# Kernel optimization log

Measured on AMD Instinct MI355X. Metric: run time of the kernel, lower is better.

Reference implementation:

```python
import jax, jax.numpy as jnp
import numpy as np

CAT = 19          # category_num + 1 (last slot is the catch-all cluster)
ATT_SCALE = float(np.sqrt(200.0))


def _layernorm(x, scale, bias, eps=1e-5):
    mu = jnp.mean(x, axis=-1, keepdims=True)
    var = jnp.mean((x - mu) ** 2, axis=-1, keepdims=True)
    return (x - mu) * jax.lax.rsqrt(var + eps) * scale + bias


def setup_inputs() -> dict:
    key = jax.random.key(0)
    ks = jax.random.split(key, 16)
    B, N, H, D, A, L = 64, 16, 100, 400, 200, 2
    nodes = H + (CAT - 1)  # 118
    s = 1.0 / np.sqrt(D)
    return {
        "history_embedding": jax.random.normal(ks[0], (B, H, D), jnp.float32),
        "candidate_news_representation": jax.random.normal(ks[1], (B, N, D), jnp.float32),
        "user_history_graph": jax.random.uniform(ks[2], (B, nodes, nodes), jnp.float32) / nodes,
        "user_history_category_mask": jax.random.randint(ks[3], (B, CAT), 0, 2, jnp.int32),
        "user_history_category_indices": jax.random.randint(ks[4], (B, H), 0, CAT, jnp.int32),
        "proxy_node_embedding": jax.random.normal(ks[5], (CAT - 1, D), jnp.float32) * 0.02,
        "gcn_W": jax.random.normal(ks[6], (L, D, D), jnp.float32) * s,
        "gcn_b": jnp.zeros((L, D), jnp.float32),
        "ln_scale": jnp.ones((L, D), jnp.float32),
        "ln_bias": jnp.zeros((L, D), jnp.float32),
        "Kw": jax.random.normal(ks[7], (D, A), jnp.float32) * s,
        "Qw": jax.random.normal(ks[8], (D, A), jnp.float32) * s,
        "Qb": jnp.zeros((A,), jnp.float32),
        "affine_W": jax.random.normal(ks[9], (D, D), jnp.float32) * s,
        "affine_b": jnp.zeros((D,), jnp.float32),
        "icKw": jax.random.normal(ks[10], (D, A), jnp.float32) * s,
        "icQw": jax.random.normal(ks[11], (D, A), jnp.float32) * s,
        "icQb": jnp.zeros((A,), jnp.float32),
    }


def _forward(history_embedding, candidate_news_representation, user_history_graph,
             proxy_node_embedding, gcn_W, gcn_b, ln_scale, ln_bias,
             Kw, Qw, Qb, affine_W, affine_b, icKw, icQw, icQb,
             user_history_category_mask, user_history_category_indices):
    B, H, D = history_embedding.shape
    N = candidate_news_representation.shape[1]
    L = gcn_W.shape[0]

    # append proxy cluster nodes to the history graph nodes (dropout = identity at eval)
    he = jnp.concatenate(
        [history_embedding, jnp.broadcast_to(proxy_node_embedding[None], (B, CAT - 1, D))],
        axis=1)  # [B, 118, D]

    # GCN with residual + layernorm per layer, then global residual
    h = he
    for l in range(L):
        z = jnp.einsum('bij,bjd->bid', user_history_graph, h) @ gcn_W[l] + gcn_b[l]
        z = jax.nn.relu(z) + h
        h = _layernorm(z, ln_scale[l], ln_bias[l])
    gcn_feat = (h + he)[:, :H]  # [B, H, D]

    # intra-cluster scatter softmax over history items grouped by category
    K = gcn_feat @ Kw                                     # [B, H, A]
    Q = candidate_news_representation @ Qw + Qb           # [B, N, A]
    a = jnp.einsum('bha,bna->bnh', K, Q) / ATT_SCALE      # [B, N, H]

    onehot = jax.nn.one_hot(user_history_category_indices, CAT, dtype=a.dtype)  # [B, H, C]
    seg = onehot.astype(bool)
    neg = jnp.finfo(a.dtype).min
    # segment-max for stable softmax: [B, N, H, C] -> max over H
    seg_max = jnp.where(seg[:, None], a[..., None], neg).max(axis=2)            # [B, N, C]
    a_shift = a - jnp.einsum('bhc,bnc->bnh', onehot, seg_max)
    e = jnp.exp(a_shift)
    denom = jnp.einsum('bhc,bnc->bnh', onehot, jnp.einsum('bnh,bhc->bnc', e, onehot))
    alpha = e / denom                                                           # [B, N, H]

    # scatter-sum of attention-weighted gcn features into category clusters
    weighted = alpha[..., None] * gcn_feat[:, None]                             # [B, N, H, D]
    intra = jnp.einsum('bnhd,bhc->bncd', weighted, onehot)                      # [B, N, C, D]
    intra = jax.nn.relu(intra @ affine_W + affine_b) + intra

    # inter-cluster scaled-dot-product candidate attention (last cluster always valid)
    mask = user_history_category_mask.at[:, -1].set(1).astype(bool)[:, None, :]  # [B, 1, C]
    Kf = intra @ icKw                                                           # [B, N, C, A]
    q = candidate_news_representation @ icQw + icQb                             # [B, N, A]
    s = jnp.einsum('bnca,bna->bnc', Kf, q) / ATT_SCALE
    w = jax.nn.softmax(jnp.where(mask, s, neg), axis=-1)
    return jnp.einsum('bnc,bncd->bnd', w, intra)                                # [B, N, D]


def reference(history_embedding, candidate_news_representation, user_history_graph,
              user_history_category_mask, user_history_category_indices,
              proxy_node_embedding, gcn_W, gcn_b, ln_scale, ln_bias,
              Kw, Qw, Qb, affine_W, affine_b, icKw, icQw, icQb):
    return _forward(history_embedding, candidate_news_representation, user_history_graph,
                    proxy_node_embedding, gcn_W, gcn_b, ln_scale, ln_bias,
                    Kw, Qw, Qb, affine_W, affine_b, icKw, icQw, icQb,
                    user_history_category_mask, user_history_category_indices)
```

## Files before the change

### kernel.cpp

```cpp
#include <hip/hip_runtime.h>
#include <hip/hip_bf16.h>
#include <math.h>

#define BB 64
#define NN 16
#define HH 100
#define DD 400
#define AA 200
#define CATN 19
#define NODES 118
#define BN (BB*NODES)
#define BH (BB*HH)
#define ATT_INV 0.07071067811865475f

typedef __attribute__((ext_vector_type(4))) float f32x4;
typedef __attribute__((ext_vector_type(8))) short s16x8;

__device__ __forceinline__ unsigned short f2bf(float f) {
  union { float f; unsigned int u; } v; v.f = f;
  unsigned int r = v.u + 0x7FFFu + ((v.u >> 16) & 1u);
  return (unsigned short)(r >> 16);
}
__device__ __forceinline__ float bf2f(unsigned short u) {
  union { unsigned int i; float f; } v; v.i = ((unsigned int)u) << 16; return v.f;
}

__global__ __launch_bounds__(256) void k_toT_he(const float* __restrict__ hist,
    const float* __restrict__ proxy, float* __restrict__ he,
    unsigned short* __restrict__ T) {
  __shared__ float t_sh[64][129];
  const int b = blockIdx.x / 7, dt = blockIdx.x % 7;
  const int d0 = dt * 64;
  const int tid = threadIdx.x;
  const int dc = tid & 63, jr = tid >> 6;
  for (int j0 = 0; j0 < 128; j0 += 4) {
    int j = j0 + jr, d = d0 + dc;
    float v = 0.f;
    if (j < NODES && d < DD) {
      v = (j < HH) ? hist[((size_t)b * HH + j) * DD + d]
                   : proxy[(size_t)(j - HH) * DD + d];
      he[((size_t)b * NODES + j) * DD + d] = v;
    }
    t_sh[dc][j] = v;
  }
  __syncthreads();
  const int jc = tid & 127, dr2 = tid >> 7;
  for (int di = 0; di < 64; di += 2) {
    int dr = di + dr2;
    int d = d0 + dr;
    if (d < 416) T[((size_t)b * 416 + d) * 128 + jc] = f2bf(t_sh[dr][jc]);
  }
}

template<int RPB>
__global__ __launch_bounds__(256) void k_toT(const float* __restrict__ h,
    unsigned short* __restrict__ T) {
  __shared__ float t_sh[64][129];
  const int b = blockIdx.x / 7, dt = blockIdx.x % 7;
  const int d0 = dt * 64;
  const int tid = threadIdx.x;
  const int dc = tid & 63, jr = tid >> 6;
  for (int j0 = 0; j0 < 128; j0 += 4) {
    int j = j0 + jr, d = d0 + dc;
    float v = (j < RPB && d < DD) ? h[((size_t)b * RPB + j) * DD + d] : 0.f;
    t_sh[dc][j] = v;
  }
  __syncthreads();
  const int jc = tid & 127, dr2 = tid >> 7;
  for (int di = 0; di < 64; di += 2) {
    int dr = di + dr2;
    int d = d0 + dr;
    if (d < 416) T[((size_t)b * 416 + d) * 128 + jc] = f2bf(t_sh[dr][jc]);
  }
}

__global__ __launch_bounds__(256) void k_toT_gf(const float* __restrict__ h2,
    const float* __restrict__ he, float* __restrict__ gf,
    unsigned short* __restrict__ T) {
  __shared__ float t_sh[64][129];
  const int b = blockIdx.x / 7, dt = blockIdx.x % 7;
  const int d0 = dt * 64;
  const int tid = threadIdx.x;
  const int dc = tid & 63, jr = tid >> 6;
  for (int j0 = 0; j0 < 128; j0 += 4) {
    int j = j0 + jr, d = d0 + dc;
    float v = 0.f;
    if (j < HH && d < DD) {
      size_t src = ((size_t)b * NODES + j) * DD + d;
      v = h2[src] + he[src];
      gf[((size_t)b * HH + j) * DD + d] = v;
    }
    t_sh[dc][j] = v;
  }
  __syncthreads();
  const int jc = tid & 127, dr2 = tid >> 7;
  for (int di = 0; di < 64; di += 2) {
    int dr = di + dr2;
    int d = d0 + dr;
    if (d < 416) T[((size_t)b * 416 + d) * 128 + jc] = f2bf(t_sh[dr][jc]);
  }
}

__global__ __launch_bounds__(256) void k_gmm(const float* __restrict__ G,
    const unsigned short* __restrict__ hT, unsigned short* __restrict__ tmpb) {
  __shared__ unsigned short a_sh[16 * 136];
  const int tid = threadIdx.x;
  const int g = (blockIdx.x & 7) * (gridDim.x >> 3) + (blockIdx.x >> 3);
  const int b = g >> 3;
  const int i0 = (g & 7) * 16;
  for (int idx = tid; idx < 16 * 128; idx += 256) {
    int r = idx >> 7, j = idx & 127;
    int i = i0 + r;
    float v = (i < NODES && j < NODES) ? G[((size_t)b * NODES + i) * NODES + j] : 0.f;
    a_sh[r * 136 + j] = f2bf(v);
  }
  __syncthreads();
  const int lane = tid & 63, w = tid >> 6;
  const int lrow = lane & 15, lk = lane >> 4;
  const int cbeg = w * 7;
  f32x4 acc[7];
#pragma unroll
  for (int c = 0; c < 7; ++c) acc[c] = f32x4{0.f, 0.f, 0.f, 0.f};
  const unsigned short* ap = &a_sh[lrow * 136 + lk * 8];
  const unsigned short* wp = &hT[((size_t)b * 416 + cbeg * 16 + lrow) * 128 + lk * 8];
  for (int ks = 0; ks < 4; ++ks) {
    s16x8 af = *reinterpret_cast<const s16x8*>(ap + ks * 32);
#pragma unroll
    for (int c = 0; c < 7; ++c) {
      s16x8 bf = *reinterpret_cast<const s16x8*>(wp + (size_t)c * 16 * 128 + ks * 32);
      acc[c] = __builtin_amdgcn_mfma_f32_16x16x32_bf16(af, bf, acc[c], 0, 0, 0);
    }
  }
#pragma unroll
  for (int c = 0; c < 7; ++c) {
    int col = (cbeg + c) * 16 + lrow;
    if (col < 416) {
#pragma unroll
      for (int j = 0; j < 4; ++j) {
        int i = i0 + lk * 4 + j;
        if (i < NODES)
          tmpb[((size_t)b * NODES + i) * 416 + col] = f2bf(acc[c][j]);
      }
    }
  }
}

__global__ __launch_bounds__(256) void k_mgb_ln(
    const unsigned short* __restrict__ A, const unsigned short* __restrict__ Wt,
    const float* __restrict__ bias, const float* __restrict__ resid,
    const float* __restrict__ lns, const float* __restrict__ lnb,
    float* __restrict__ out) {
  __shared__ float ps_sh[16][4][2];
  const int tid = threadIdx.x;
  const int g = (blockIdx.x % 8) * (gridDim.x / 8) + blockIdx.x / 8;
  const size_t row0 = (size_t)g * 16;
  const int lane = tid & 63, w = tid >> 6;
  const int lrow = lane & 15, lk = lane >> 4;
  const int cbeg = w * 7;
  f32x4 acc[7];
#pragma unroll
  for (int c = 0; c < 7; ++c) acc[c] = f32x4{0.f, 0.f, 0.f, 0.f};
  const unsigned short* ap = &A[(row0 + lrow) * 416 + lk * 8];
  const unsigned short* wp = &Wt[((size_t)(cbeg * 16) + lrow) * 416 + lk * 8];
  for (int ks = 0; ks < 13; ++ks) {
    s16x8 af = *reinterpret_cast<const s16x8*>(ap + ks * 32);
#pragma unroll
    for (int c = 0; c < 7; ++c) {
      s16x8 bf = *reinterpret_cast<const s16x8*>(wp + (size_t)c * 16 * 416 + ks * 32);
      acc[c] = __builtin_amdgcn_mfma_f32_16x16x32_bf16(af, bf, acc[c], 0, 0, 0);
    }
  }
  float zs[4], zq[4];
#pragma unroll
  for (int j = 0; j < 4; ++j) { zs[j] = 0.f; zq[j] = 0.f; }
#pragma unroll
  for (int c = 0; c < 7; ++c) {
    int col = (cbeg + c) * 16 + lrow;
    bool cv = col < DD;
    float bv = cv ? bias[col] : 0.f;
#pragma unroll
    for (int j = 0; j < 4; ++j) {
      float z = 0.f;
      if (cv)
        z = fmaxf(acc[c][j] + bv, 0.f) + resid[(row0 + lk * 4 + j) * (size_t)DD + col];
      acc[c][j] = z;
      zs[j] += z;
      zq[j] += z * z;
    }
  }
#pragma unroll
  for (int j = 0; j < 4; ++j) {
    zs[j] += __shfl_xor(zs[j], 1, 64); zq[j] += __shfl_xor(zq[j], 1, 64);
    zs[j] += __shfl_xor(zs[j], 2, 64); zq[j] += __shfl_xor(zq[j], 2, 64);
    zs[j] += __shfl_xor(zs[j], 4, 64); zq[j] += __shfl_xor(zq[j], 4, 64);
    zs[j] += __shfl_xor(zs[j], 8, 64); zq[j] += __shfl_xor(zq[j], 8, 64);
  }
  if (lrow == 0) {
#pragma unroll
    for (int j = 0; j < 4; ++j) {
      ps_sh[lk * 4 + j][w][0] = zs[j];
      ps_sh[lk * 4 + j][w][1] = zq[j];
    }
  }
  __syncthreads();
  float mu[4], rs[4];
#pragma unroll
  for (int j = 0; j < 4; ++j) {
    int la = lk * 4 + j;
    float s = ps_sh[la][0][0] + ps_sh[la][1][0] + ps_sh[la][2][0] + ps_sh[la][3][0];
    float q = ps_sh[la][0][1] + ps_sh[la][1][1] + ps_sh[la][2][1] + ps_sh[la][3][1];
    mu[j] = s * (1.0f / DD);
    rs[j] = 1.0f / sqrtf(q * (1.0f / DD) - mu[j] * mu[j] + 1e-5f);
  }
#pragma unroll
  for (int c = 0; c < 7; ++c) {
    int col = (cbeg + c) * 16 + lrow;
    if (col < DD) {
      float sc = lns[col], bo = lnb[col];
#pragma unroll
      for (int j = 0; j < 4; ++j)
        out[(row0 + lk * 4 + j) * (size_t)DD + col] = (acc[c][j] - mu[j]) * rs[j] * sc + bo;
    }
  }
}

__global__ __launch_bounds__(256) void k_prep_all(const float* __restrict__ gW,
    const float* __restrict__ afW, const float* __restrict__ Kw,
    const float* __restrict__ Qw, const float* __restrict__ icQw,
    const float* __restrict__ icKw, const float* __restrict__ Qb,
    const float* __restrict__ icQb, unsigned short* __restrict__ wbase,
    float* __restrict__ bias3) {
  int idx = blockIdx.x * 256 + threadIdx.x;
  const int SG = 416 * 416;
  const int SK = 224 * 416;
  if (idx < SG) {
    int n = idx / 416, k = idx - n * 416;
    wbase[idx] = (n < 400 && k < 400) ? f2bf(gW[(size_t)k * 400 + n]) : (unsigned short)0;
    return;
  }
  idx -= SG;
  if (idx < SG) {
    int n = idx / 416, k = idx - n * 416;
    wbase[173056 + idx] = (n < 400 && k < 400) ? f2bf(gW[160000 + (size_t)k * 400 + n]) : (unsigned short)0;
    return;
  }
  idx -= SG;
  if (idx < SG) {
    int n = idx / 416, k = idx - n * 416;
    wbase[346112 + idx] = (n < 400 && k < 400) ? f2bf(afW[(size_t)k * 400 + n]) : (unsigned short)0;
    return;
  }
  idx -= SG;
  if (idx < SK) {
    int n = idx / 416, k = idx - n * 416;
    wbase[519168 + idx] = (n < 200 && k < 400) ? f2bf(Kw[(size_t)k * 200 + n]) : (unsigned short)0;
    return;
  }
  idx -= SK;
  if (idx < SK) {
    int d = idx / 224, a = idx - d * 224;
    wbase[612352 + idx] = (d < 400 && a < 200) ? f2bf(icKw[(size_t)d * 200 + a]) : (unsigned short)0;
    return;
  }
  idx -= SK;
  if (idx < SK) {
    int k = idx / 224, a = idx - k * 224;
    wbase[705536 + idx] = (k < 400 && a < 200) ? f2bf(icQw[(size_t)k * 200 + a]) : (unsigned short)0;
    return;
  }
  idx -= SK;
  if (idx < 208 * 416) {
    int n = idx / 416, k = idx - n * 416;
    wbase[798720 + idx] = (n < 200 && k < 400) ? f2bf(Qw[(size_t)k * 200 + n]) : (unsigned short)0;
    return;
  }
  idx -= 208 * 416;
  if (idx < 608) {
    float v = 0.f;
    if (idx < 200) v = Qb[idx];
    else if (idx >= 208) {
      const float* kr = icKw + (size_t)(idx - 208) * 200;
      float s = 0.f;
      for (int a = 0; a < 200; ++a) s += icQb[a] * kr[a];
      v = s;
    }
    bias3[idx] = v;
  }
}

__global__ __launch_bounds__(256) void k_prep_M(const unsigned short* __restrict__ icKwB,
    const unsigned short* __restrict__ icQwB, unsigned short* __restrict__ wqp) {
  const int tid = threadIdx.x;
  const size_t row0 = (size_t)blockIdx.x * 32;
  const int lane = tid & 63, w = tid >> 6;
  const int lrow = lane & 15, lk = lane >> 4;
  const int rg = w & 1, nh = w >> 1;
  const int cbeg = nh * 13;
  f32x4 acc[13];
#pragma unroll
  for (int c = 0; c < 13; ++c) acc[c] = f32x4{0.f, 0.f, 0.f, 0.f};
  const unsigned short* ap = &icKwB[(row0 + rg * 16 + lrow) * 224 + lk * 8];
  const unsigned short* bp = &icQwB[((size_t)(cbeg * 16) + lrow) * 224 + lk * 8];
  for (int ks = 0; ks < 7; ++ks) {
    s16x8 af = *reinterpret_cast<const s16x8*>(ap + ks * 32);
#pragma unroll
    for (int c = 0; c < 13; ++c) {
      s16x8 bf = *reinterpret_cast<const s16x8*>(bp + (size_t)c * 16 * 224 + ks * 32);
      acc[c] = __builtin_amdgcn_mfma_f32_16x16x32_bf16(af, bf, acc[c], 0, 0, 0);
    }
  }
  const int r0 = rg * 16 + lk * 4;
#pragma unroll
  for (int c = 0; c < 13; ++c) {
    int k = (cbeg + c) * 16 + lrow;
#pragma unroll
    for (int j = 0; j < 4; ++j) {
      size_t d = row0 + r0 + j;
      if (d < 400) wqp[(208 + d) * 416 + k] = f2bf(acc[c][j]);
    }
  }
}

template<int KDIM, int KPAD, int NOUT, int EPI>
__global__ __launch_bounds__(256) void k_mg(
    const float* __restrict__ A, const unsigned short* __restrict__ Wt,
    const float* __restrict__ bias, float* __restrict__ out, float* __restrict__ out2) {
  constexpr int APITCH = KPAD + 8;
  constexpr int NF = (NOUT + 15) / 16;
  constexpr int NF0 = (NF + 1) / 2;
  constexpr int KS = KPAD / 32;
  constexpr int E4 = KDIM / 4;
  constexpr int PADN = KPAD - KDIM;
  __shared__ unsigned short a_sh[32 * APITCH];
  const int tid = threadIdx.x;
  const int g = (blockIdx.x % 8) * (gridDim.x / 8) + blockIdx.x / 8;
  const size_t row0 = (size_t)g * 32;
  for (int i = tid; i < 32 * E4; i += 256) {
    int r = i / E4, c4 = i - r * E4;
    const float4 v = *reinterpret_cast<const float4*>(&A[(row0 + r) * (size_t)KDIM + c4 * 4]);
    unsigned int lo = (unsigned int)f2bf(v.x) | ((unsigned int)f2bf(v.y) << 16);
    unsigned int hi = (unsigned int)f2bf(v.z) | ((unsigned int)f2bf(v.w) << 16);
    *reinterpret_cast<uint2*>(&a_sh[r * APITCH + c4 * 4]) = make_uint2(lo, hi);
  }
  for (int i = tid; i < 32 * PADN; i += 256) {
    int r = i / PADN, c = i - r * PADN;
    a_sh[r * APITCH + KDIM + c] = 0;
  }
  __syncthreads();
  const int lane = tid & 63, w = tid >> 6;
  const int lrow = lane & 15, lk = lane >> 4;
  const int rg = w & 1, nh = w >> 1;
  const int cbeg = nh * NF0;
  f32x4 acc[NF0];
#pragma unroll
  for (int c = 0; c < NF0; ++c) acc[c] = f32x4{0.f, 0.f, 0.f, 0.f};
  const unsigned short* ap = &a_sh[(rg * 16 + lrow) * APITCH + lk * 8];
  const unsigned short* wp = &Wt[((size_t)(cbeg * 16) + lrow) * KPAD + lk * 8];
  for (int ks = 0; ks < KS; ++ks) {
    s16x8 af = *reinterpret_cast<const s16x8*>(ap + ks * 32);
#pragma unroll
    for (int c = 0; c < NF0; ++c) {
      s16x8 bf = *reinterpret_cast<const s16x8*>(wp + (size_t)c * 16 * KPAD + ks * 32);
      acc[c] = __builtin_amdgcn_mfma_f32_16x16x32_bf16(af, bf, acc[c], 0, 0, 0);
    }
  }
  const int r0 = rg * 16 + lk * 4;
  if (EPI == 0) {
#pragma unroll
    for (int c = 0; c < NF0; ++c) {
      int col = (cbeg + c) * 16 + lrow;
      if (col < NOUT) {
#pragma unroll
        for (int j = 0; j < 4; ++j)
          out[(row0 + r0 + j) * (size_t)NOUT + col] = acc[c][j];
      }
    }
  } else {
#pragma unroll
    for (int c = 0; c < NF0; ++c) {
      int col = (cbeg + c) * 16 + lrow;
      if (col < 200) {
        float bv = bias[col];
#pragma unroll
        for (int j = 0; j < 4; ++j)
          out[(row0 + r0 + j) * (size_t)AA + col] = acc[c][j] + bv;
      } else if (col >= 208 && col < 608) {
        float bv = bias[col];
#pragma unroll
        for (int j = 0; j < 4; ++j)
          out2[(row0 + r0 + j) * (size_t)DD + (col - 208)] = acc[c][j] + bv;
      }
    }
  }
}

__global__ __launch_bounds__(256) void k_palpha(const float* __restrict__ K,
    const float* __restrict__ Q, const int* __restrict__ cat,
    unsigned short* __restrict__ P) {
  __shared__ float q_sh[AA];
  __shared__ float a_sh[HH];
  __shared__ int c_sh[HH];
  __shared__ float smax[CATN], sden[CATN];
  const int i = blockIdx.x;
  const int xcd = i & 7, s = i >> 3;
  const int b = 8 * xcd + (s >> 4);
  const int n = s & 15;
  const int bn = b * 16 + n;
  const int tid = threadIdx.x;
  if (tid < AA) q_sh[tid] = Q[(size_t)bn * AA + tid];
  if (tid < HH) c_sh[tid] = cat[b * HH + tid];
  __syncthreads();
  if (tid < 2 * HH) {
    int h = tid >> 1, half = tid & 1;
    const float* kp = K + ((size_t)b * HH + h) * AA + half * 100;
    const float* qp = q_sh + half * 100;
    float sv = 0.f;
#pragma unroll 4
    for (int a = 0; a < 100; ++a) sv += kp[a] * qp[a];
    sv += __shfl_xor(sv, 1, 64);
    if (half == 0) a_sh[h] = sv * ATT_INV;
  }
  __syncthreads();
  if (tid < CATN) {
    float m = -3.4e38f;
    for (int h = 0; h < HH; ++h)
      if (c_sh[h] == tid) m = fmaxf(m, a_sh[h]);
    smax[tid] = m;
  }
  __syncthreads();
  if (tid < HH) a_sh[tid] = expf(a_sh[tid] - smax[c_sh[tid]]);
  __syncthreads();
  if (tid < CATN) {
    float dsum = 0.f;
    for (int h = 0; h < HH; ++h)
      if (c_sh[h] == tid) dsum += a_sh[h];
    sden[tid] = dsum;
  }
  __syncthreads();
  if (tid < HH) a_sh[tid] = a_sh[tid] / sden[c_sh[tid]];
  __syncthreads();
  for (int idx = tid; idx < CATN * 128; idx += 256) {
    int c = idx >> 7, h = idx & 127;
    float v = (h < HH && c_sh[h] == c) ? a_sh[h] : 0.f;
    P[((size_t)b * 320 + n * CATN + c) * 128 + h] = f2bf(v);
  }
}

__global__ __launch_bounds__(256) void k_sc(const unsigned short* __restrict__ P,
    const unsigned short* __restrict__ gfT, unsigned short* __restrict__ intraB) {
  const int i = blockIdx.x;
  const int xcd = i & 7, s = i >> 3;
  const int b = 8 * xcd + s / CATN;
  const int t = s % CATN;
  const int tid = threadIdx.x;
  const int lane = tid & 63, w = tid >> 6;
  const int lrow = lane & 15, lk = lane >> 4;
  const int cbeg = w * 7;
  f32x4 acc[7];
#pragma unroll
  for (int c = 0; c < 7; ++c) acc[c] = f32x4{0.f, 0.f, 0.f, 0.f};
  const unsigned short* ap = &P[((size_t)b * 320 + t * 16 + lrow) * 128 + lk * 8];
  const unsigned short* wp = &gfT[((size_t)b * 416 + cbeg * 16 + lrow) * 128 + lk * 8];
  for (int ks = 0; ks < 4; ++ks) {
    s16x8 af = *reinterpret_cast<const s16x8*>(ap + ks * 32);
#pragma unroll
    for (int c = 0; c < 7; ++c) {
      s16x8 bf = *reinterpret_cast<const s16x8*>(wp + (size_t)c * 16 * 128 + ks * 32);
      acc[c] = __builtin_amdgcn_mfma_f32_16x16x32_bf16(af, bf, acc[c], 0, 0, 0);
    }
  }
#pragma unroll
  for (int c = 0; c < 7; ++c) {
    int col = (cbeg + c) * 16 + lrow;
    if (col < 416) {
#pragma unroll
      for (int j = 0; j < 4; ++j)
        intraB[((size_t)b * 304 + t * 16 + lk * 4 + j) * 416 + col] =
            f2bf(col < DD ? acc[c][j] : 0.f);
    }
  }
}

__global__ __launch_bounds__(256) void k_afq(
    const unsigned short* __restrict__ A, const unsigned short* __restrict__ Wt,
    const float* __restrict__ bias, const float* __restrict__ p,
    float* __restrict__ s_pre, unsigned short* __restrict__ out2) {
  __shared__ float ps_sh[16][4];
  const int tid = threadIdx.x;
  const int g = (blockIdx.x % 8) * (gridDim.x / 8) + blockIdx.x / 8;
  const size_t row0 = (size_t)g * 16;
  const int lane = tid & 63, w = tid >> 6;
  const int lrow = lane & 15, lk = lane >> 4;
  const int cbeg = w * 7;
  f32x4 acc[7];
#pragma unroll
  for (int c = 0; c < 7; ++c) acc[c] = f32x4{0.f, 0.f, 0.f, 0.f};
  const unsigned short* ap = &A[(row0 + lrow) * 416 + lk * 8];
  const unsigned short* wp = &Wt[((size_t)(cbeg * 16) + lrow) * 416 + lk * 8];
  for (int ks = 0; ks < 13; ++ks) {
    s16x8 af = *reinterpret_cast<const s16x8*>(ap + ks * 32);
#pragma unroll
    for (int c = 0; c < 7; ++c) {
      s16x8 bf = *reinterpret_cast<const s16x8*>(wp + (size_t)c * 16 * 416 + ks * 32);
      acc[c] = __builtin_amdgcn_mfma_f32_16x16x32_bf16(af, bf, acc[c], 0, 0, 0);
    }
  }
  const float* prow[4];
#pragma unroll
  for (int j = 0; j < 4; ++j)
    prow[j] = p + (size_t)((row0 + lk * 4 + j) / CATN) * DD;
  float sp[4] = {0.f, 0.f, 0.f, 0.f};
#pragma unroll
  for (int c = 0; c < 7; ++c) {
    int col = (cbeg + c) * 16 + lrow;
    if (col < DD) {
      float bv = bias[col];
#pragma unroll
      for (int j = 0; j < 4; ++j) {
        size_t ra = row0 + lk * 4 + j;
        float v = fmaxf(acc[c][j] + bv, 0.f) + bf2f(A[ra * 416 + col]);
        out2[ra * 416 + col] = f2bf(v);
        sp[j] += v * prow[j][col];
      }
    }
  }
#pragma unroll
  for (int j = 0; j < 4; ++j) {
    sp[j] += __shfl_xor(sp[j], 1, 64);
    sp[j] += __shfl_xor(sp[j], 2, 64);
    sp[j] += __shfl_xor(sp[j], 4, 64);
    sp[j] += __shfl_xor(sp[j], 8, 64);
  }
  if (lrow == 0) {
#pragma unroll
    for (int j = 0; j < 4; ++j) ps_sh[lk * 4 + j][w] = sp[j];
  }
  __syncthreads();
  if (tid < 16)
    s_pre[row0 + tid] =
        (ps_sh[tid][0] + ps_sh[tid][1] + ps_sh[tid][2] + ps_sh[tid][3]) * ATT_INV;
}

__global__ __launch_bounds__(256) void k_final(const unsigned short* __restrict__ intra2B,
    const float* __restrict__ s_pre, const int* __restrict__ mask,
    float* __restrict__ out) {
  __shared__ float w_sh[CATN];
  const int i = blockIdx.x;
  const int xcd = i & 7, s = i >> 3;
  const int b = 8 * xcd + (s >> 4);
  const int n = s & 15;
  const int bn = b * 16 + n;
  const int tid = threadIdx.x;
  if (tid == 0) {
    float sv[CATN];
    float mx = -3.4e38f;
#pragma unroll
    for (int c = 0; c < CATN; ++c) {
      bool mk = (c == CATN - 1) || (mask[b * CATN + c] != 0);
      float sc = mk ? s_pre[bn * CATN + c] : -3.4e38f;
      sv[c] = sc;
      mx = fmaxf(mx, sc);
    }
    float den = 0.f;
#pragma unroll
    for (int c = 0; c < CATN; ++c) {
      float e = (sv[c] <= -3.3e38f) ? 0.f : expf(sv[c] - mx);
      w_sh[c] = e;
      den += e;
    }
    float inv = 1.0f / den;
#pragma unroll
    for (int c = 0; c < CATN; ++c) w_sh[c] *= inv;
  }
  __syncthreads();
  const unsigned short* ib = intra2B + (size_t)bn * CATN * 416;
  for (int d = tid; d < DD; d += 256) {
    float o = 0.f;
#pragma unroll
    for (int c = 0; c < CATN; ++c) o += w_sh[c] * bf2f(ib[c * 416 + d]);
    out[(size_t)bn * DD + d] = o;
  }
}

extern "C" void kernel_launch(void* const* d_in, const int* in_sizes, int n_in,
                              void* d_out, int out_size, void* d_ws, size_t ws_size,
                              hipStream_t stream) {
  const float* hist  = (const float*)d_in[0];
  const float* cand  = (const float*)d_in[1];
  const float* G     = (const float*)d_in[2];
  const int*   cmask = (const int*)d_in[3];
  const int*   cidx  = (const int*)d_in[4];
  const float* proxy = (const float*)d_in[5];
  const float* gW    = (const float*)d_in[6];
  const float* gb    = (const float*)d_in[7];
  const float* lns   = (const float*)d_in[8];
  const float* lnb   = (const float*)d_in[9];
  const float* Kw    = (const float*)d_in[10];
  const float* Qw    = (const float*)d_in[11];
  const float* Qbb   = (const float*)d_in[12];
  const float* afW   = (const float*)d_in[13];
  const float* afb   = (const float*)d_in[14];
  const float* icKw  = (const float*)d_in[15];
  const float* icQw  = (const float*)d_in[16];
  const float* icQb  = (const float*)d_in[17];
  float* out = (float*)d_out;
  float* ws  = (float*)d_ws;

  float* he    = ws;
  float* s1    = ws + 3020800;
  float* s2f   = ws + 6041600;
  unsigned short* tmpb   = (unsigned short*)(ws + 6041600);
  unsigned short* TB     = (unsigned short*)(ws + 9062400);
  unsigned short* intraB = (unsigned short*)(ws + 10766336);
  unsigned short* intra2B= (unsigned short*)(ws + 14813184);
  unsigned short* wbase  = (unsigned short*)(ws + 18860032);
  float* bias3 = ws + 19385856;
  unsigned short* Pbuf = (unsigned short*)ws;
  float* qbuf  = ws + 1310720;
  float* pbuf  = ws + 1515520;
  float* s_pre = ws + 1925120;
  float* Kbuf  = s1;
  unsigned short* gW0t  = wbase;
  unsigned short* gW1t  = wbase + 173056;
  unsigned short* afWt  = wbase + 346112;
  unsigned short* Kwt   = wbase + 519168;
  unsigned short* icKwB = wbase + 612352;
  unsigned short* icQwB = wbase + 705536;
  unsigned short* Wqp   = wbase + 798720;

  k_prep_all<<<3461, 256, 0, stream>>>(gW, afW, Kw, Qw, icQw, icKw, Qbb, icQb, wbase, bias3);
  k_prep_M<<<13, 256, 0, stream>>>(icKwB, icQwB, Wqp);
  k_toT_he<<<448, 256, 0, stream>>>(hist, proxy, he, TB);
  k_gmm<<<512, 256, 0, stream>>>(G, TB, tmpb);
  k_mgb_ln<<<BN / 16, 256, 0, stream>>>(tmpb, gW0t, gb, he, lns, lnb, s1);
  k_toT<NODES><<<448, 256, 0, stream>>>(s1, TB);
  k_gmm<<<512, 256, 0, stream>>>(G, TB, tmpb);
  k_mgb_ln<<<BN / 16, 256, 0, stream>>>(tmpb, gW1t, gb + DD, s1, lns + DD, lnb + DD, s1);
  k_toT_gf<<<448, 256, 0, stream>>>(s1, he, s2f, TB);
  k_mg<400, 416, 200, 0><<<BH / 32, 256, 0, stream>>>(s2f, Kwt, nullptr, Kbuf, nullptr);
  k_mg<400, 416, 608, 6><<<BB * NN / 32, 256, 0, stream>>>(cand, Wqp, bias3, qbuf, pbuf);
  k_palpha<<<BB * NN, 256, 0, stream>>>(Kbuf, qbuf, cidx, Pbuf);
  k_sc<<<BB * CATN, 256, 0, stream>>>(Pbuf, TB, intraB);
  k_afq<<<BB * NN * CATN / 16, 256, 0, stream>>>(intraB, afWt, afb, pbuf, s_pre, intra2B);
  k_final<<<BB * NN, 256, 0, stream>>>(intra2B, s_pre, cmask, out);
}
```

Measured before the change: 311.5 us.

## Fuse transposed bf16 writes into GCN LayerNorm epilogue; retile small GEMMs to 16 rows

Removes the standalone transpose kernels (k_toT, k_toT_gf). The LayerNorm GEMM epilogue now writes the transposed bf16 copy directly, and in the second layer also adds the residual to produce the graph features. The K/Q projection GEMMs switch to 16-row tiles with each wave owning a column slice, which doubles block count for better occupancy, and the padded weight tail is zero-filled. The fused transposed stores are scattered 2-byte writes with a stride of 128 elements, so they are poorly coalesced compared with the shared-memory transpose they replace.

```diff
diff --git a/kernel.cpp b/kernel.cpp
--- a/kernel.cpp
+++ b/kernel.cpp
@@ -52,55 +52,6 @@
   }
 }
 
-template<int RPB>
-__global__ __launch_bounds__(256) void k_toT(const float* __restrict__ h,
-    unsigned short* __restrict__ T) {
-  __shared__ float t_sh[64][129];
-  const int b = blockIdx.x / 7, dt = blockIdx.x % 7;
-  const int d0 = dt * 64;
-  const int tid = threadIdx.x;
-  const int dc = tid & 63, jr = tid >> 6;
-  for (int j0 = 0; j0 < 128; j0 += 4) {
-    int j = j0 + jr, d = d0 + dc;
-    float v = (j < RPB && d < DD) ? h[((size_t)b * RPB + j) * DD + d] : 0.f;
-    t_sh[dc][j] = v;
-  }
-  __syncthreads();
-  const int jc = tid & 127, dr2 = tid >> 7;
-  for (int di = 0; di < 64; di += 2) {
-    int dr = di + dr2;
-    int d = d0 + dr;
-    if (d < 416) T[((size_t)b * 416 + d) * 128 + jc] = f2bf(t_sh[dr][jc]);
-  }
-}
-
-__global__ __launch_bounds__(256) void k_toT_gf(const float* __restrict__ h2,
-    const float* __restrict__ he, float* __restrict__ gf,
-    unsigned short* __restrict__ T) {
-  __shared__ float t_sh[64][129];
-  const int b = blockIdx.x / 7, dt = blockIdx.x % 7;
-  const int d0 = dt * 64;
-  const int tid = threadIdx.x;
-  const int dc = tid & 63, jr = tid >> 6;
-  for (int j0 = 0; j0 < 128; j0 += 4) {
-    int j = j0 + jr, d = d0 + dc;
-    float v = 0.f;
-    if (j < HH && d < DD) {
-      size_t src = ((size_t)b * NODES + j) * DD + d;
-      v = h2[src] + he[src];
-      gf[((size_t)b * HH + j) * DD + d] = v;
-    }
-    t_sh[dc][j] = v;
-  }
-  __syncthreads();
-  const int jc = tid & 127, dr2 = tid >> 7;
-  for (int di = 0; di < 64; di += 2) {
-    int dr = di + dr2;
-    int d = d0 + dr;
-    if (d < 416) T[((size_t)b * 416 + d) * 128 + jc] = f2bf(t_sh[dr][jc]);
-  }
-}
-
 __global__ __launch_bounds__(256) void k_gmm(const float* __restrict__ G,
     const unsigned short* __restrict__ hT, unsigned short* __restrict__ tmpb) {
   __shared__ unsigned short a_sh[16 * 136];
@@ -145,11 +96,13 @@
   }
 }
 
+template<int MODE>
 __global__ __launch_bounds__(256) void k_mgb_ln(
     const unsigned short* __restrict__ A, const unsigned short* __restrict__ Wt,
     const float* __restrict__ bias, const float* __restrict__ resid,
     const float* __restrict__ lns, const float* __restrict__ lnb,
-    float* __restrict__ out) {
+    float* __restrict__ out, unsigned short* __restrict__ T,
+    const float* __restrict__ he) {
   __shared__ float ps_sh[16][4][2];
   const int tid = threadIdx.x;
   const int g = (blockIdx.x % 8) * (gridDim.x / 8) + blockIdx.x / 8;
@@ -218,8 +171,24 @@
     if (col < DD) {
       float sc = lns[col], bo = lnb[col];
 #pragma unroll
-      for (int j = 0; j < 4; ++j)
-        out[(row0 + lk * 4 + j) * (size_t)DD + col] = (acc[c][j] - mu[j]) * rs[j] * sc + bo;
+      for (int j = 0; j < 4; ++j) {
+        size_t row = row0 + lk * 4 + j;
+        int b = (int)(row / NODES);
+        int i = (int)(row - (size_t)b * NODES);
+        float v = (acc[c][j] - mu[j]) * rs[j] * sc + bo;
+        if (MODE == 0) {
+          out[row * (size_t)DD + col] = v;
+          T[((size_t)b * 416 + col) * 128 + i] = f2bf(v);
+        } else {
+          if (i < HH) {
+            float gg = v + he[row * (size_t)DD + col];
+            out[((size_t)b * HH + i) * (size_t)DD + col] = gg;
+            T[((size_t)b * 416 + col) * 128 + i] = f2bf(gg);
+          } else {
+            T[((size_t)b * 416 + col) * 128 + i] = 0;
+          }
+        }
+      }
     }
   }
 }
@@ -275,6 +244,11 @@
     return;
   }
   idx -= 208 * 416;
+  if (idx < 32 * 416) {
+    wbase[798720 + 608 * 416 + idx] = 0;
+    return;
+  }
+  idx -= 32 * 416;
   if (idx < 608) {
     float v = 0.f;
     if (idx < 200) v = Qb[idx];
@@ -321,74 +295,70 @@
   }
 }
 
-template<int KDIM, int KPAD, int NOUT, int EPI>
-__global__ __launch_bounds__(256) void k_mg(
+template<int KDIM, int KPAD, int NOUT, int NFW, int EPI>
+__global__ __launch_bounds__(256) void k_mg16(
     const float* __restrict__ A, const unsigned short* __restrict__ Wt,
     const float* __restrict__ bias, float* __restrict__ out, float* __restrict__ out2) {
   constexpr int APITCH = KPAD + 8;
-  constexpr int NF = (NOUT + 15) / 16;
-  constexpr int NF0 = (NF + 1) / 2;
-  constexpr int KS = KPAD / 32;
   constexpr int E4 = KDIM / 4;
   constexpr int PADN = KPAD - KDIM;
-  __shared__ unsigned short a_sh[32 * APITCH];
+  constexpr int KS = KPAD / 32;
+  __shared__ unsigned short a_sh[16 * APITCH];
   const int tid = threadIdx.x;
   const int g = (blockIdx.x % 8) * (gridDim.x / 8) + blockIdx.x / 8;
-  const size_t row0 = (size_t)g * 32;
-  for (int i = tid; i < 32 * E4; i += 256) {
+  const size_t row0 = (size_t)g * 16;
+  for (int i = tid; i < 16 * E4; i += 256) {
     int r = i / E4, c4 = i - r * E4;
     const float4 v = *reinterpret_cast<const float4*>(&A[(row0 + r) * (size_t)KDIM + c4 * 4]);
     unsigned int lo = (unsigned int)f2bf(v.x) | ((unsigned int)f2bf(v.y) << 16);
     unsigned int hi = (unsigned int)f2bf(v.z) | ((unsigned int)f2bf(v.w) << 16);
     *reinterpret_cast<uint2*>(&a_sh[r * APITCH + c4 * 4]) = make_uint2(lo, hi);
   }
-  for (int i = tid; i < 32 * PADN; i += 256) {
+  for (int i = tid; i < 16 * PADN; i += 256) {
     int r = i / PADN, c = i - r * PADN;
     a_sh[r * APITCH + KDIM + c] = 0;
   }
   __syncthreads();
   const int lane = tid & 63, w = tid >> 6;
   const int lrow = lane & 15, lk = lane >> 4;
-  const int rg = w & 1, nh = w >> 1;
-  const int cbeg = nh * NF0;
-  f32x4 acc[NF0];
-#pragma unroll
-  for (int c = 0; c < NF0; ++c) acc[c] = f32x4{0.f, 0.f, 0.f, 0.f};
-  const unsigned short* ap = &a_sh[(rg * 16 + lrow) * APITCH + lk * 8];
+  const int cbeg = w * NFW;
+  f32x4 acc[NFW];
+#pragma unroll
+  for (int c = 0; c < NFW; ++c) acc[c] = f32x4{0.f, 0.f, 0.f, 0.f};
+  const unsigned short* ap = &a_sh[lrow * APITCH + lk * 8];
   const unsigned short* wp = &Wt[((size_t)(cbeg * 16) + lrow) * KPAD + lk * 8];
   for (int ks = 0; ks < KS; ++ks) {
     s16x8 af = *reinterpret_cast<const s16x8*>(ap + ks * 32);
 #pragma unroll
-    for (int c = 0; c < NF0; ++c) {
+    for (int c = 0; c < NFW; ++c) {
       s16x8 bf = *reinterpret_cast<const s16x8*>(wp + (size_t)c * 16 * KPAD + ks * 32);
       acc[c] = __builtin_amdgcn_mfma_f32_16x16x32_bf16(af, bf, acc[c], 0, 0, 0);
     }
   }
-  const int r0 = rg * 16 + lk * 4;
   if (EPI == 0) {
 #pragma unroll
-    for (int c = 0; c < NF0; ++c) {
+    for (int c = 0; c < NFW; ++c) {
       int col = (cbeg + c) * 16 + lrow;
       if (col < NOUT) {
 #pragma unroll
         for (int j = 0; j < 4; ++j)
-          out[(row0 + r0 + j) * (size_t)NOUT + col] = acc[c][j];
+          out[(row0 + lk * 4 + j) * (size_t)NOUT + col] = acc[c][j];
       }
     }
   } else {
 #pragma unroll
-    for (int c = 0; c < NF0; ++c) {
+    for (int c = 0; c < NFW; ++c) {
       int col = (cbeg + c) * 16 + lrow;
       if (col < 200) {
         float bv = bias[col];
 #pragma unroll
         for (int j = 0; j < 4; ++j)
-          out[(row0 + r0 + j) * (size_t)AA + col] = acc[c][j] + bv;
+          out[(row0 + lk * 4 + j) * (size_t)AA + col] = acc[c][j] + bv;
       } else if (col >= 208 && col < 608) {
         float bv = bias[col];
 #pragma unroll
         for (int j = 0; j < 4; ++j)
-          out2[(row0 + r0 + j) * (size_t)DD + (col - 208)] = acc[c][j] + bv;
+          out2[(row0 + lk * 4 + j) * (size_t)DD + (col - 208)] = acc[c][j] + bv;
       }
     }
   }
@@ -608,13 +578,13 @@
 
   float* he    = ws;
   float* s1    = ws + 3020800;
-  float* s2f   = ws + 6041600;
   unsigned short* tmpb   = (unsigned short*)(ws + 6041600);
   unsigned short* TB     = (unsigned short*)(ws + 9062400);
+  float* gf    = ws + 10766336;
   unsigned short* intraB = (unsigned short*)(ws + 10766336);
   unsigned short* intra2B= (unsigned short*)(ws + 14813184);
   unsigned short* wbase  = (unsigned short*)(ws + 18860032);
-  float* bias3 = ws + 19385856;
+  float* bias3 = ws + 19392512;
   unsigned short* Pbuf = (unsigned short*)ws;
   float* qbuf  = ws + 1310720;
   float* pbuf  = ws + 1515520;
@@ -628,17 +598,15 @@
   unsigned short* icQwB = wbase + 705536;
   unsigned short* Wqp   = wbase + 798720;
 
-  k_prep_all<<<3461, 256, 0, stream>>>(gW, afW, Kw, Qw, icQw, icKw, Qbb, icQb, wbase, bias3);
+  k_prep_all<<<3513, 256, 0, stream>>>(gW, afW, Kw, Qw, icQw, icKw, Qbb, icQb, wbase, bias3);
   k_prep_M<<<13, 256, 0, stream>>>(icKwB, icQwB, Wqp);
   k_toT_he<<<448, 256, 0, stream>>>(hist, proxy, he, TB);
   k_gmm<<<512, 256, 0, stream>>>(G, TB, tmpb);
-  k_mgb_ln<<<BN / 16, 256, 0, stream>>>(tmpb, gW0t, gb, he, lns, lnb, s1);
-  k_toT<NODES><<<448, 256, 0, stream>>>(s1, TB);
+  k_mgb_ln<0><<<BN / 16, 256, 0, stream>>>(tmpb, gW0t, gb, he, lns, lnb, s1, TB, nullptr);
   k_gmm<<<512, 256, 0, stream>>>(G, TB, tmpb);
-  k_mgb_ln<<<BN / 16, 256, 0, stream>>>(tmpb, gW1t, gb + DD, s1, lns + DD, lnb + DD, s1);
-  k_toT_gf<<<448, 256, 0, stream>>>(s1, he, s2f, TB);
-  k_mg<400, 416, 200, 0><<<BH / 32, 256, 0, stream>>>(s2f, Kwt, nullptr, Kbuf, nullptr);
-  k_mg<400, 416, 608, 6><<<BB * NN / 32, 256, 0, stream>>>(cand, Wqp, bias3, qbuf, pbuf);
+  k_mgb_ln<1><<<BN / 16, 256, 0, stream>>>(tmpb, gW1t, gb + DD, s1, lns + DD, lnb + DD, gf, TB, he);
+  k_mg16<400, 416, 200, 4, 0><<<BH / 16, 256, 0, stream>>>(gf, Kwt, nullptr, Kbuf, nullptr);
+  k_mg16<400, 416, 608, 10, 6><<<BB * NN / 16, 256, 0, stream>>>(cand, Wqp, bias3, qbuf, pbuf);
   k_palpha<<<BB * NN, 256, 0, stream>>>(Kbuf, qbuf, cidx, Pbuf);
   k_sc<<<BB * CATN, 256, 0, stream>>>(Pbuf, TB, intraB);
   k_afq<<<BB * NN * CATN / 16, 256, 0, stream>>>(intraB, afWt, afb, pbuf, s_pre, intra2B);
```

Result: faster. 290.3 us, median of 2 (-6.8%).
